# Performance work log

Hardware: AMD Instinct MI355X
Metric: run time of the kernel (lower is better)

Reference implementation:

```python
import math
import jax, jax.numpy as jnp
import numpy as np

NUM_HEADS = 8
D_EMBED = 512
D_HEAD = D_EMBED // NUM_HEADS


def setup_inputs() -> dict:
    key = jax.random.key(0)
    k1, k2, k3, k4, k5 = jax.random.split(key, 5)
    B, S = 1, 4096
    scale_in = 1.0 / math.sqrt(D_EMBED)
    return {
        "x": jax.random.normal(k1, (B, S, D_EMBED), dtype=jnp.float32),
        "w_in": jax.random.normal(k2, (3 * D_EMBED, D_EMBED), dtype=jnp.float32) * scale_in,
        "b_in": jax.random.normal(k3, (3 * D_EMBED,), dtype=jnp.float32) * 0.01,
        "w_out": jax.random.normal(k4, (D_EMBED, D_EMBED), dtype=jnp.float32) * scale_in,
        "b_out": jax.random.normal(k5, (D_EMBED,), dtype=jnp.float32) * 0.01,
        "causal_mask": 0,
    }


def reference(x, w_in, b_in, w_out, b_out, causal_mask):
    B, S, D = x.shape
    # in_proj: torch Linear => x @ W^T + b, then chunk into Q,K,V
    qkv = x @ w_in.T + b_in                      # (B, S, 3D)
    q, k, v = jnp.split(qkv, 3, axis=-1)
    def heads(t):
        return t.reshape(B, S, NUM_HEADS, D_HEAD).transpose(0, 2, 1, 3)  # (B,H,S,Dh)
    q, k, v = heads(q), heads(k), heads(v)
    scores = jnp.einsum("bhqd,bhkd->bhqk", q, k)  # (B,H,S,S)
    if bool(causal_mask):
        mask = jnp.triu(jnp.ones((S, S), dtype=bool), 1)
        scores = jnp.where(mask, -jnp.inf, scores)
    scores = scores / math.sqrt(D_HEAD)
    # NOTE: faithful to the source, softmax is over dim=1 (the HEADS axis)
    w = jax.nn.softmax(scores, axis=1)
    out = jnp.einsum("bhqk,bhkd->bhqd", w, v)    # (B,H,S,Dh)
    out = out.transpose(0, 2, 1, 3).reshape(B, S, D)
    return out @ w_out.T + b_out
```

## Files before the change

kernel.cpp:

```cpp
#include <hip/hip_runtime.h>
#include <hip/hip_bf16.h>

typedef __bf16 bf16_t;
typedef __bf16 bf16x8 __attribute__((ext_vector_type(8)));
typedef __bf16 bf16x4 __attribute__((ext_vector_type(4)));
typedef float  f32x4  __attribute__((ext_vector_type(4)));

#define S_LEN 4096
#define NH    8
#define DH    64
#define DE    512

#define BM 128
#define BN 128
#define BK 32
#define LDP 40

static __device__ __forceinline__ void stage16_f32(bf16_t* dst, const float* src) {
    const float4 v0 = *reinterpret_cast<const float4*>(src + 0);
    const float4 v1 = *reinterpret_cast<const float4*>(src + 4);
    const float4 v2 = *reinterpret_cast<const float4*>(src + 8);
    const float4 v3 = *reinterpret_cast<const float4*>(src + 12);
    bf16x8 lo, hi;
    lo[0]=(bf16_t)v0.x; lo[1]=(bf16_t)v0.y; lo[2]=(bf16_t)v0.z; lo[3]=(bf16_t)v0.w;
    lo[4]=(bf16_t)v1.x; lo[5]=(bf16_t)v1.y; lo[6]=(bf16_t)v1.z; lo[7]=(bf16_t)v1.w;
    hi[0]=(bf16_t)v2.x; hi[1]=(bf16_t)v2.y; hi[2]=(bf16_t)v2.z; hi[3]=(bf16_t)v2.w;
    hi[4]=(bf16_t)v3.x; hi[5]=(bf16_t)v3.y; hi[6]=(bf16_t)v3.z; hi[7]=(bf16_t)v3.w;
    *reinterpret_cast<bf16x8*>(dst + 0) = lo;
    *reinterpret_cast<bf16x8*>(dst + 8) = hi;
}

__global__ __launch_bounds__(256) void qkv_gemm(
    const float* __restrict__ X,
    const float* __restrict__ Win,
    const float* __restrict__ bin,
    bf16_t* __restrict__ qw,
    bf16_t* __restrict__ kw,
    bf16_t* __restrict__ vtw)
{
    __shared__ bf16_t As[BM * LDP];
    __shared__ bf16_t Bs[BN * LDP];

    const int tid  = threadIdx.x;
    const int lane = tid & 63;
    const int w    = tid >> 6;
    const int wr   = w >> 1, wc = w & 1;
    const int row0 = blockIdx.y * BM;
    const int col0 = blockIdx.x * BN;

    const int fr = lane & 15;
    const int fo = (lane >> 4) * 8;
    const int cr = (lane >> 4) * 4;

    const int sr = tid >> 1;
    const int sc = (tid & 1) * 16;

    f32x4 acc[4][4] = {};

    for (int k0 = 0; k0 < DE; k0 += BK) {
        stage16_f32(As + sr * LDP + sc, X   + (row0 + sr) * DE + k0 + sc);
        stage16_f32(Bs + sr * LDP + sc, Win + (col0 + sr) * DE + k0 + sc);
        __syncthreads();

        bf16x8 af[4], bf[4];
        #pragma unroll
        for (int m = 0; m < 4; ++m)
            af[m] = *reinterpret_cast<const bf16x8*>(As + (wr * 64 + m * 16 + fr) * LDP + fo);
        #pragma unroll
        for (int n = 0; n < 4; ++n)
            bf[n] = *reinterpret_cast<const bf16x8*>(Bs + (wc * 64 + n * 16 + fr) * LDP + fo);
        #pragma unroll
        for (int m = 0; m < 4; ++m)
            #pragma unroll
            for (int n = 0; n < 4; ++n)
                acc[m][n] = __builtin_amdgcn_mfma_f32_16x16x32_bf16(af[m], bf[n], acc[m][n], 0, 0, 0);
        __syncthreads();
    }

    #pragma unroll
    for (int m = 0; m < 4; ++m) {
        #pragma unroll
        for (int n = 0; n < 4; ++n) {
            const int col = col0 + wc * 64 + n * 16 + fr;
            const float b = bin[col];
            const int part = col >> 9;
            const int cd   = col & 511;
            const int h    = cd >> 6;
            const int d    = cd & 63;
            #pragma unroll
            for (int r = 0; r < 4; ++r) {
                const int row = row0 + wr * 64 + m * 16 + cr + r;
                const float v = acc[m][n][r] + b;
                const bf16_t bv = (bf16_t)v;
                if (part == 0)      qw [(h * S_LEN + row) * DH + d] = bv;
                else if (part == 1) kw [(h * S_LEN + row) * DH + d] = bv;
                else                vtw[(h * DH + d) * S_LEN + row] = bv;
            }
        }
    }
}

template<int QT, int KS>
__global__ __launch_bounds__(512, 4) void attn_kernel(
    const bf16_t* __restrict__ qw,
    const bf16_t* __restrict__ kw,
    const bf16_t* __restrict__ vtw,
    const int*    __restrict__ causal_p,
    bf16_t* __restrict__ part)
{
    constexpr int QF = QT / 16;
    constexpr int NT = (S_LEN / KS) / 64;
    constexpr int KSH = (KS == 4) ? 2 : (KS == 2 ? 1 : 0);

    __shared__ bf16_t e_lds[2][NH][QT][64];

    const int tid  = threadIdx.x;
    const int lane = tid & 63;
    const int h    = tid >> 6;
    const int kc   = blockIdx.x & (KS - 1);
    const int q0   = (blockIdx.x >> KSH) * QT;
    const int kbase = kc * (S_LEN / KS);
    const int causal = causal_p[0];

    const int fr  = lane & 15;
    const int fog = lane >> 4;
    const int fo  = fog * 8;
    const int cr  = fog * 4;

    bf16x8 aq[QF][2];
    #pragma unroll
    for (int qf = 0; qf < QF; ++qf) {
        const bf16_t* qb = qw + ((size_t)(h * S_LEN) + q0 + qf * 16 + fr) * DH;
        aq[qf][0] = *reinterpret_cast<const bf16x8*>(qb + fo);
        aq[qf][1] = *reinterpret_cast<const bf16x8*>(qb + 32 + fo);
    }

    f32x4 o[QF][4] = {};

    for (int t = 0; t < NT; ++t) {
        const int kg = kbase + t * 64;
        bf16_t* wbuf = &e_lds[t & 1][h][0][0];

        #pragma unroll 1
        for (int kf = 0; kf < 4; ++kf) {
            const bf16_t* kb = kw + ((size_t)(h * S_LEN) + kg + kf * 16 + fr) * DH;
            const bf16x8 b0 = *reinterpret_cast<const bf16x8*>(kb + fo);
            const bf16x8 b1 = *reinterpret_cast<const bf16x8*>(kb + 32 + fo);
            #pragma unroll
            for (int qf = 0; qf < QF; ++qf) {
                f32x4 z = {};
                z = __builtin_amdgcn_mfma_f32_16x16x32_bf16(aq[qf][0], b0, z, 0, 0, 0);
                z = __builtin_amdgcn_mfma_f32_16x16x32_bf16(aq[qf][1], b1, z, 0, 0, 0);
                #pragma unroll
                for (int r = 0; r < 4; ++r) {
                    float val = __expf(z[r] * 0.125f);
                    if (causal) {
                        if (kg + kf * 16 + fr > q0 + qf * 16 + cr + r) val = 0.f;
                    }
                    const int q = qf * 16 + cr + r;
                    const int k = kf * 16 + fr;
                    const int bp = (k >> 3) ^ (q & 7);
                    wbuf[q * 64 + bp * 8 + (k & 7)] = (bf16_t)val;
                }
            }
        }

        __syncthreads();

        if (tid < QT * 16) {
            const int q  = tid >> 4;
            const int hb = tid & 15;
            const int bp = (hb >> 1) ^ (q & 7);
            bf16_t* base = &e_lds[t & 1][0][0][0] + q * 64 + bp * 8 + (hb & 1) * 4;

            float den0 = 0.f, den1 = 0.f, den2 = 0.f, den3 = 0.f;
            #pragma unroll
            for (int hh = 0; hh < NH; ++hh) {
                const bf16x4 v = *reinterpret_cast<const bf16x4*>(base + hh * (QT * 64));
                den0 += (float)v[0]; den1 += (float)v[1];
                den2 += (float)v[2]; den3 += (float)v[3];
            }
            const float rd0 = (den0 > 0.f) ? __builtin_amdgcn_rcpf(den0) : 0.f;
            const float rd1 = (den1 > 0.f) ? __builtin_amdgcn_rcpf(den1) : 0.f;
            const float rd2 = (den2 > 0.f) ? __builtin_amdgcn_rcpf(den2) : 0.f;
            const float rd3 = (den3 > 0.f) ? __builtin_amdgcn_rcpf(den3) : 0.f;
            #pragma unroll
            for (int hh = 0; hh < NH; ++hh) {
                bf16_t* p = base + hh * (QT * 64);
                const bf16x4 v = *reinterpret_cast<const bf16x4*>(p);
                bf16x4 wv;
                wv[0] = (bf16_t)((float)v[0] * rd0);
                wv[1] = (bf16_t)((float)v[1] * rd1);
                wv[2] = (bf16_t)((float)v[2] * rd2);
                wv[3] = (bf16_t)((float)v[3] * rd3);
                *reinterpret_cast<bf16x4*>(p) = wv;
            }
        }
        __syncthreads();

        #pragma unroll 1
        for (int c = 0; c < 2; ++c) {
            bf16x8 pa[QF];
            #pragma unroll
            for (int qf = 0; qf < QF; ++qf) {
                const int q  = qf * 16 + fr;
                const int bp = (4 * c + fog) ^ (q & 7);
                pa[qf] = *reinterpret_cast<const bf16x8*>(wbuf + q * 64 + bp * 8);
            }
            #pragma unroll
            for (int n = 0; n < 4; ++n) {
                const bf16x8 vvn = *reinterpret_cast<const bf16x8*>(
                    vtw + ((size_t)(h * DH + n * 16 + fr)) * S_LEN + kg + c * 32 + fo);
                #pragma unroll
                for (int qf = 0; qf < QF; ++qf)
                    o[qf][n] = __builtin_amdgcn_mfma_f32_16x16x32_bf16(pa[qf], vvn, o[qf][n], 0, 0, 0);
            }
        }
    }

    bf16_t* pp = part + (size_t)kc * (S_LEN * DE);
    #pragma unroll
    for (int qf = 0; qf < QF; ++qf)
        #pragma unroll
        for (int n = 0; n < 4; ++n)
            #pragma unroll
            for (int r = 0; r < 4; ++r)
                pp[(size_t)(q0 + qf * 16 + cr + r) * DE + h * 64 + n * 16 + fr] =
                    (bf16_t)o[qf][n][r];
}

template<int KS>
__global__ __launch_bounds__(256) void out_gemm(
    const bf16_t* __restrict__ part,
    const float*  __restrict__ Wout,
    const float*  __restrict__ bout,
    float* __restrict__ out)
{
    __shared__ bf16_t As[BM * LDP];
    __shared__ bf16_t Bs[BN * LDP];

    const int tid  = threadIdx.x;
    const int lane = tid & 63;
    const int w    = tid >> 6;
    const int wr   = w >> 1, wc = w & 1;
    const int row0 = blockIdx.y * BM;
    const int col0 = blockIdx.x * BN;

    const int fr = lane & 15;
    const int fo = (lane >> 4) * 8;
    const int cr = (lane >> 4) * 4;

    const int sr = tid >> 1;
    const int sc = (tid & 1) * 16;

    f32x4 acc[4][4] = {};

    for (int k0 = 0; k0 < DE; k0 += BK) {
        {
            const size_t off = (size_t)(row0 + sr) * DE + k0 + sc;
            #pragma unroll
            for (int v = 0; v < 2; ++v) {
                bf16x8 a = *reinterpret_cast<const bf16x8*>(part + off + v * 8);
                #pragma unroll
                for (int p = 1; p < KS; ++p) {
                    bf16x8 b = *reinterpret_cast<const bf16x8*>(
                        part + (size_t)p * (S_LEN * DE) + off + v * 8);
                    #pragma unroll
                    for (int j = 0; j < 8; ++j)
                        a[j] = (bf16_t)((float)a[j] + (float)b[j]);
                }
                *reinterpret_cast<bf16x8*>(As + sr * LDP + sc + v * 8) = a;
            }
        }
        stage16_f32(Bs + sr * LDP + sc, Wout + (col0 + sr) * DE + k0 + sc);
        __syncthreads();

        bf16x8 af[4], bf[4];
        #pragma unroll
        for (int m = 0; m < 4; ++m)
            af[m] = *reinterpret_cast<const bf16x8*>(As + (wr * 64 + m * 16 + fr) * LDP + fo);
        #pragma unroll
        for (int n = 0; n < 4; ++n)
            bf[n] = *reinterpret_cast<const bf16x8*>(Bs + (wc * 64 + n * 16 + fr) * LDP + fo);
        #pragma unroll
        for (int m = 0; m < 4; ++m)
            #pragma unroll
            for (int n = 0; n < 4; ++n)
                acc[m][n] = __builtin_amdgcn_mfma_f32_16x16x32_bf16(af[m], bf[n], acc[m][n], 0, 0, 0);
        __syncthreads();
    }

    #pragma unroll
    for (int m = 0; m < 4; ++m) {
        #pragma unroll
        for (int n = 0; n < 4; ++n) {
            const int col = col0 + wc * 64 + n * 16 + fr;
            const float b = bout[col];
            #pragma unroll
            for (int r = 0; r < 4; ++r) {
                const int row = row0 + wr * 64 + m * 16 + cr + r;
                out[row * DE + col] = acc[m][n][r] + b;
            }
        }
    }
}

extern "C" void kernel_launch(void* const* d_in, const int* in_sizes, int n_in,
                              void* d_out, int out_size, void* d_ws, size_t ws_size,
                              hipStream_t stream) {
    const float* x     = (const float*)d_in[0];
    const float* w_in  = (const float*)d_in[1];
    const float* b_in  = (const float*)d_in[2];
    const float* w_out = (const float*)d_in[3];
    const float* b_out = (const float*)d_in[4];
    const int*   causal = (const int*)d_in[5];
    float* out = (float*)d_out;

    const size_t segE = (size_t)NH * S_LEN * DH;
    bf16_t* qw   = (bf16_t*)d_ws;
    bf16_t* kw   = qw  + segE;
    bf16_t* vtw  = kw  + segE;
    bf16_t* part = vtw + segE;

    dim3 g1(3 * DE / BN, S_LEN / BM);
    qkv_gemm<<<g1, 256, 0, stream>>>(x, w_in, b_in, qw, kw, vtw);

    dim3 g3(DE / BN, S_LEN / BM);

    const size_t segB = segE * sizeof(bf16_t);
    if (ws_size >= 7 * segB) {
        attn_kernel<32, 4><<<512, 512, 0, stream>>>(qw, kw, vtw, causal, part);
        out_gemm<4><<<g3, 256, 0, stream>>>(part, w_out, b_out, out);
    } else if (ws_size >= 5 * segB) {
        attn_kernel<32, 2><<<256, 512, 0, stream>>>(qw, kw, vtw, causal, part);
        out_gemm<2><<<g3, 256, 0, stream>>>(part, w_out, b_out, out);
    } else {
        attn_kernel<16, 1><<<256, 512, 0, stream>>>(qw, kw, vtw, causal, part);
        out_gemm<1><<<g3, 256, 0, stream>>>(part, w_out, b_out, out);
    }
}
```

Measured before the change: 193.2 us.

## Split attention query tile across two waves per head with 1024-thread blocks

The attention kernel now runs 16 waves per block, two per head, and each wave handles 16 of the 32 query rows instead of all 32. QK^T operands are swapped so each lane holds four consecutive keys for one query, which lets the exp values go to LDS as one packed bf16x4 store. The cross-head normalization pass now uses all 1024 threads on bf16x2 pairs. The goal is more waves in flight to hide latency and fewer scalar LDS writes. In exchange, K and V tiles are loaded twice per head (once per wave) and the larger blocks with launch bounds (1024, 2) may limit occupancy.

```diff
diff --git a/kernel.cpp b/kernel.cpp
--- a/kernel.cpp
+++ b/kernel.cpp
@@ -4,6 +4,7 @@
 typedef __bf16 bf16_t;
 typedef __bf16 bf16x8 __attribute__((ext_vector_type(8)));
 typedef __bf16 bf16x4 __attribute__((ext_vector_type(4)));
+typedef __bf16 bf16x2 __attribute__((ext_vector_type(2)));
 typedef float  f32x4  __attribute__((ext_vector_type(4)));
 
 #define S_LEN 4096
@@ -100,15 +101,15 @@
     }
 }
 
-template<int QT, int KS>
-__global__ __launch_bounds__(512, 4) void attn_kernel(
+template<int KS>
+__global__ __launch_bounds__(1024, 2) void attn_kernel(
     const bf16_t* __restrict__ qw,
     const bf16_t* __restrict__ kw,
     const bf16_t* __restrict__ vtw,
     const int*    __restrict__ causal_p,
     bf16_t* __restrict__ part)
 {
-    constexpr int QF = QT / 16;
+    constexpr int QT = 32;
     constexpr int NT = (S_LEN / KS) / 64;
     constexpr int KSH = (KS == 4) ? 2 : (KS == 2 ? 1 : 0);
 
@@ -116,7 +117,9 @@
 
     const int tid  = threadIdx.x;
     const int lane = tid & 63;
-    const int h    = tid >> 6;
+    const int wid  = tid >> 6;
+    const int h    = wid & 7;
+    const int qh   = wid >> 3;
     const int kc   = blockIdx.x & (KS - 1);
     const int q0   = (blockIdx.x >> KSH) * QT;
     const int kbase = kc * (S_LEN / KS);
@@ -126,107 +129,91 @@
     const int fog = lane >> 4;
     const int fo  = fog * 8;
     const int cr  = fog * 4;
-
-    bf16x8 aq[QF][2];
-    #pragma unroll
-    for (int qf = 0; qf < QF; ++qf) {
-        const bf16_t* qb = qw + ((size_t)(h * S_LEN) + q0 + qf * 16 + fr) * DH;
-        aq[qf][0] = *reinterpret_cast<const bf16x8*>(qb + fo);
-        aq[qf][1] = *reinterpret_cast<const bf16x8*>(qb + 32 + fo);
-    }
-
-    f32x4 o[QF][4] = {};
+    const int qw0 = qh * 16;
+
+    bf16x8 aq0, aq1;
+    {
+        const bf16_t* qb = qw + ((size_t)(h * S_LEN) + q0 + qw0 + fr) * DH;
+        aq0 = *reinterpret_cast<const bf16x8*>(qb + fo);
+        aq1 = *reinterpret_cast<const bf16x8*>(qb + 32 + fo);
+    }
+
+    f32x4 o[4] = {};
 
     for (int t = 0; t < NT; ++t) {
         const int kg = kbase + t * 64;
-        bf16_t* wbuf = &e_lds[t & 1][h][0][0];
+        bf16_t* ebuf = &e_lds[t & 1][h][0][0];
 
         #pragma unroll 1
         for (int kf = 0; kf < 4; ++kf) {
             const bf16_t* kb = kw + ((size_t)(h * S_LEN) + kg + kf * 16 + fr) * DH;
-            const bf16x8 b0 = *reinterpret_cast<const bf16x8*>(kb + fo);
-            const bf16x8 b1 = *reinterpret_cast<const bf16x8*>(kb + 32 + fo);
-            #pragma unroll
-            for (int qf = 0; qf < QF; ++qf) {
-                f32x4 z = {};
-                z = __builtin_amdgcn_mfma_f32_16x16x32_bf16(aq[qf][0], b0, z, 0, 0, 0);
-                z = __builtin_amdgcn_mfma_f32_16x16x32_bf16(aq[qf][1], b1, z, 0, 0, 0);
-                #pragma unroll
-                for (int r = 0; r < 4; ++r) {
-                    float val = __expf(z[r] * 0.125f);
-                    if (causal) {
-                        if (kg + kf * 16 + fr > q0 + qf * 16 + cr + r) val = 0.f;
-                    }
-                    const int q = qf * 16 + cr + r;
-                    const int k = kf * 16 + fr;
-                    const int bp = (k >> 3) ^ (q & 7);
-                    wbuf[q * 64 + bp * 8 + (k & 7)] = (bf16_t)val;
+            const bf16x8 k0v = *reinterpret_cast<const bf16x8*>(kb + fo);
+            const bf16x8 k1v = *reinterpret_cast<const bf16x8*>(kb + 32 + fo);
+            f32x4 z = {};
+            z = __builtin_amdgcn_mfma_f32_16x16x32_bf16(k0v, aq0, z, 0, 0, 0);
+            z = __builtin_amdgcn_mfma_f32_16x16x32_bf16(k1v, aq1, z, 0, 0, 0);
+            bf16x4 ev;
+            #pragma unroll
+            for (int r = 0; r < 4; ++r) {
+                float val = __expf(z[r] * 0.125f);
+                if (causal) {
+                    if (kg + kf * 16 + cr + r > q0 + qw0 + fr) val = 0.f;
                 }
-            }
-        }
-
-        __syncthreads();
-
-        if (tid < QT * 16) {
-            const int q  = tid >> 4;
-            const int hb = tid & 15;
-            const int bp = (hb >> 1) ^ (q & 7);
-            bf16_t* base = &e_lds[t & 1][0][0][0] + q * 64 + bp * 8 + (hb & 1) * 4;
-
-            float den0 = 0.f, den1 = 0.f, den2 = 0.f, den3 = 0.f;
+                ev[r] = (bf16_t)val;
+            }
+            const int q = qw0 + fr;
+            const int p = (kf * 2 + (fog >> 1)) ^ (fr & 7);
+            *reinterpret_cast<bf16x4*>(ebuf + q * 64 + p * 8 + (fog & 1) * 4) = ev;
+        }
+
+        __syncthreads();
+
+        {
+            const int q = tid >> 5;
+            const int j = tid & 31;
+            const int p = (j >> 2) ^ (q & 7);
+            bf16_t* base = &e_lds[t & 1][0][0][0] + q * 64 + p * 8 + (j & 3) * 2;
+            float d0 = 0.f, d1 = 0.f;
             #pragma unroll
             for (int hh = 0; hh < NH; ++hh) {
-                const bf16x4 v = *reinterpret_cast<const bf16x4*>(base + hh * (QT * 64));
-                den0 += (float)v[0]; den1 += (float)v[1];
-                den2 += (float)v[2]; den3 += (float)v[3];
-            }
-            const float rd0 = (den0 > 0.f) ? __builtin_amdgcn_rcpf(den0) : 0.f;
-            const float rd1 = (den1 > 0.f) ? __builtin_amdgcn_rcpf(den1) : 0.f;
-            const float rd2 = (den2 > 0.f) ? __builtin_amdgcn_rcpf(den2) : 0.f;
-            const float rd3 = (den3 > 0.f) ? __builtin_amdgcn_rcpf(den3) : 0.f;
+                const bf16x2 v = *reinterpret_cast<const bf16x2*>(base + hh * (QT * 64));
+                d0 += (float)v[0]; d1 += (float)v[1];
+            }
+            const float r0 = (d0 > 0.f) ? __builtin_amdgcn_rcpf(d0) : 0.f;
+            const float r1 = (d1 > 0.f) ? __builtin_amdgcn_rcpf(d1) : 0.f;
             #pragma unroll
             for (int hh = 0; hh < NH; ++hh) {
-                bf16_t* p = base + hh * (QT * 64);
-                const bf16x4 v = *reinterpret_cast<const bf16x4*>(p);
-                bf16x4 wv;
-                wv[0] = (bf16_t)((float)v[0] * rd0);
-                wv[1] = (bf16_t)((float)v[1] * rd1);
-                wv[2] = (bf16_t)((float)v[2] * rd2);
-                wv[3] = (bf16_t)((float)v[3] * rd3);
-                *reinterpret_cast<bf16x4*>(p) = wv;
+                bf16_t* pp = base + hh * (QT * 64);
+                const bf16x2 v = *reinterpret_cast<const bf16x2*>(pp);
+                bf16x2 wv;
+                wv[0] = (bf16_t)((float)v[0] * r0);
+                wv[1] = (bf16_t)((float)v[1] * r1);
+                *reinterpret_cast<bf16x2*>(pp) = wv;
             }
         }
         __syncthreads();
 
         #pragma unroll 1
         for (int c = 0; c < 2; ++c) {
-            bf16x8 pa[QF];
-            #pragma unroll
-            for (int qf = 0; qf < QF; ++qf) {
-                const int q  = qf * 16 + fr;
-                const int bp = (4 * c + fog) ^ (q & 7);
-                pa[qf] = *reinterpret_cast<const bf16x8*>(wbuf + q * 64 + bp * 8);
-            }
+            const int q = qw0 + fr;
+            const int p = (c * 4 + fog) ^ (fr & 7);
+            const bf16x8 pa = *reinterpret_cast<const bf16x8*>(ebuf + q * 64 + p * 8);
             #pragma unroll
             for (int n = 0; n < 4; ++n) {
                 const bf16x8 vvn = *reinterpret_cast<const bf16x8*>(
                     vtw + ((size_t)(h * DH + n * 16 + fr)) * S_LEN + kg + c * 32 + fo);
-                #pragma unroll
-                for (int qf = 0; qf < QF; ++qf)
-                    o[qf][n] = __builtin_amdgcn_mfma_f32_16x16x32_bf16(pa[qf], vvn, o[qf][n], 0, 0, 0);
+                o[n] = __builtin_amdgcn_mfma_f32_16x16x32_bf16(pa, vvn, o[n], 0, 0, 0);
             }
         }
     }
 
     bf16_t* pp = part + (size_t)kc * (S_LEN * DE);
     #pragma unroll
-    for (int qf = 0; qf < QF; ++qf)
-        #pragma unroll
-        for (int n = 0; n < 4; ++n)
-            #pragma unroll
-            for (int r = 0; r < 4; ++r)
-                pp[(size_t)(q0 + qf * 16 + cr + r) * DE + h * 64 + n * 16 + fr] =
-                    (bf16_t)o[qf][n][r];
+    for (int n = 0; n < 4; ++n)
+        #pragma unroll
+        for (int r = 0; r < 4; ++r)
+            pp[(size_t)(q0 + qw0 + cr + r) * DE + h * 64 + n * 16 + fr] =
+                (bf16_t)o[n][r];
 }
 
 template<int KS>
@@ -329,13 +316,13 @@
 
     const size_t segB = segE * sizeof(bf16_t);
     if (ws_size >= 7 * segB) {
-        attn_kernel<32, 4><<<512, 512, 0, stream>>>(qw, kw, vtw, causal, part);
+        attn_kernel<4><<<512, 1024, 0, stream>>>(qw, kw, vtw, causal, part);
         out_gemm<4><<<g3, 256, 0, stream>>>(part, w_out, b_out, out);
     } else if (ws_size >= 5 * segB) {
-        attn_kernel<32, 2><<<256, 512, 0, stream>>>(qw, kw, vtw, causal, part);
+        attn_kernel<2><<<256, 1024, 0, stream>>>(qw, kw, vtw, causal, part);
         out_gemm<2><<<g3, 256, 0, stream>>>(part, w_out, b_out, out);
     } else {
-        attn_kernel<16, 1><<<256, 512, 0, stream>>>(qw, kw, vtw, causal, part);
+        attn_kernel<1><<<128, 1024, 0, stream>>>(qw, kw, vtw, causal, part);
         out_gemm<1><<<g3, 256, 0, stream>>>(part, w_out, b_out, out);
     }
 }
```

Result: slower. 323.9 us (+67.7%).

## Prefetch next K tile into registers and use LDS-only barriers in attention loop

Applied to the files above, without the earlier changes.

Loads the K fragments for the next 64-key tile into registers before the barrier, so global load latency overlaps the head-softmax normalization and PV stage. Replaces __syncthreads with a custom barrier that waits only on LDS counters, leaving the global prefetch in flight across barriers. The PV stage is also unrolled to load both P chunks up front. Costs extra VGPRs for the prefetch buffers and unrolled loops, which may lower occupancy.

```diff
diff --git a/kernel.cpp b/kernel.cpp
--- a/kernel.cpp
+++ b/kernel.cpp
@@ -30,6 +30,12 @@
     *reinterpret_cast<bf16x8*>(dst + 8) = hi;
 }
 
+static __device__ __forceinline__ void bar_lds() {
+    __builtin_amdgcn_sched_barrier(0);
+    asm volatile("s_waitcnt lgkmcnt(0)\n\ts_barrier" ::: "memory");
+    __builtin_amdgcn_sched_barrier(0);
+}
+
 __global__ __launch_bounds__(256) void qkv_gemm(
     const float* __restrict__ X,
     const float* __restrict__ Win,
@@ -137,20 +143,28 @@
 
     f32x4 o[QF][4] = {};
 
+    bf16x8 kA[4], kB[4];
+    {
+        #pragma unroll
+        for (int kf = 0; kf < 4; ++kf) {
+            const bf16_t* kb = kw + ((size_t)(h * S_LEN) + kbase + kf * 16 + fr) * DH;
+            kA[kf] = *reinterpret_cast<const bf16x8*>(kb + fo);
+            kB[kf] = *reinterpret_cast<const bf16x8*>(kb + 32 + fo);
+        }
+    }
+
+    #pragma unroll 1
     for (int t = 0; t < NT; ++t) {
         const int kg = kbase + t * 64;
         bf16_t* wbuf = &e_lds[t & 1][h][0][0];
 
-        #pragma unroll 1
+        #pragma unroll
         for (int kf = 0; kf < 4; ++kf) {
-            const bf16_t* kb = kw + ((size_t)(h * S_LEN) + kg + kf * 16 + fr) * DH;
-            const bf16x8 b0 = *reinterpret_cast<const bf16x8*>(kb + fo);
-            const bf16x8 b1 = *reinterpret_cast<const bf16x8*>(kb + 32 + fo);
             #pragma unroll
             for (int qf = 0; qf < QF; ++qf) {
                 f32x4 z = {};
-                z = __builtin_amdgcn_mfma_f32_16x16x32_bf16(aq[qf][0], b0, z, 0, 0, 0);
-                z = __builtin_amdgcn_mfma_f32_16x16x32_bf16(aq[qf][1], b1, z, 0, 0, 0);
+                z = __builtin_amdgcn_mfma_f32_16x16x32_bf16(aq[qf][0], kA[kf], z, 0, 0, 0);
+                z = __builtin_amdgcn_mfma_f32_16x16x32_bf16(aq[qf][1], kB[kf], z, 0, 0, 0);
                 #pragma unroll
                 for (int r = 0; r < 4; ++r) {
                     float val = __expf(z[r] * 0.125f);
@@ -165,7 +179,17 @@
             }
         }
 
-        __syncthreads();
+        if (t + 1 < NT) {
+            const int kn = kg + 64;
+            #pragma unroll
+            for (int kf = 0; kf < 4; ++kf) {
+                const bf16_t* kb = kw + ((size_t)(h * S_LEN) + kn + kf * 16 + fr) * DH;
+                kA[kf] = *reinterpret_cast<const bf16x8*>(kb + fo);
+                kB[kf] = *reinterpret_cast<const bf16x8*>(kb + 32 + fo);
+            }
+        }
+
+        bar_lds();
 
         if (tid < QT * 16) {
             const int q  = tid >> 4;
@@ -196,25 +220,28 @@
                 *reinterpret_cast<bf16x4*>(p) = wv;
             }
         }
-        __syncthreads();
-
-        #pragma unroll 1
-        for (int c = 0; c < 2; ++c) {
-            bf16x8 pa[QF];
-            #pragma unroll
-            for (int qf = 0; qf < QF; ++qf) {
-                const int q  = qf * 16 + fr;
-                const int bp = (4 * c + fog) ^ (q & 7);
-                pa[qf] = *reinterpret_cast<const bf16x8*>(wbuf + q * 64 + bp * 8);
-            }
-            #pragma unroll
-            for (int n = 0; n < 4; ++n) {
-                const bf16x8 vvn = *reinterpret_cast<const bf16x8*>(
-                    vtw + ((size_t)(h * DH + n * 16 + fr)) * S_LEN + kg + c * 32 + fo);
+        bar_lds();
+
+        {
+            bf16x8 pa[2][QF];
+            #pragma unroll
+            for (int c = 0; c < 2; ++c)
                 #pragma unroll
-                for (int qf = 0; qf < QF; ++qf)
-                    o[qf][n] = __builtin_amdgcn_mfma_f32_16x16x32_bf16(pa[qf], vvn, o[qf][n], 0, 0, 0);
-            }
+                for (int qf = 0; qf < QF; ++qf) {
+                    const int q  = qf * 16 + fr;
+                    const int bp = (4 * c + fog) ^ (q & 7);
+                    pa[c][qf] = *reinterpret_cast<const bf16x8*>(wbuf + q * 64 + bp * 8);
+                }
+            #pragma unroll
+            for (int c = 0; c < 2; ++c)
+                #pragma unroll
+                for (int n = 0; n < 4; ++n) {
+                    const bf16x8 vvn = *reinterpret_cast<const bf16x8*>(
+                        vtw + ((size_t)(h * DH + n * 16 + fr)) * S_LEN + kg + c * 32 + fo);
+                    #pragma unroll
+                    for (int qf = 0; qf < QF; ++qf)
+                        o[qf][n] = __builtin_amdgcn_mfma_f32_16x16x32_bf16(pa[c][qf], vvn, o[qf][n], 0, 0, 0);
+                }
         }
     }
 
```

New measurement: 356.2 us. 84.4% more time.
